# Kernel tuning notes

Measured on AMD Instinct MI355X. Metric: run time of the kernel, lower is better.

## Reference

```python
import jax, jax.numpy as jnp
import numpy as np
from functools import partial


def conv2d(x, w, b, pad):
    # x: [B,C,H,W], w: [O,I,kh,kw]
    out = jax.lax.conv_general_dilated(
        x, w, window_strides=(1, 1), padding=[(pad, pad), (pad, pad)],
        dimension_numbers=("NCHW", "OIHW", "NCHW"))
    return out + b[None, :, None, None]


def maxpool3x3_s1(x):
    return jax.lax.reduce_window(
        x, -jnp.inf, jax.lax.max, (1, 1, 3, 3), (1, 1, 1, 1),
        padding=((0, 0), (0, 0), (1, 1), (1, 1)))


def bilinear_sample(img, y, x):
    # img: [B,C,H,W]; y, x: [B,H,W] float sample coords. Zero outside bounds.
    def one(im, yy, xx):  # im [C,H,W]
        H, W = im.shape[1], im.shape[2]
        y0 = jnp.floor(yy)
        x0 = jnp.floor(xx)
        wy = yy - y0
        wx = xx - x0
        y0i = y0.astype(jnp.int32)
        x0i = x0.astype(jnp.int32)

        def g(yi, xi):
            valid = (yi >= 0) & (yi < H) & (xi >= 0) & (xi < W)
            yc = jnp.clip(yi, 0, H - 1)
            xc = jnp.clip(xi, 0, W - 1)
            return im[:, yc, xc] * valid[None].astype(im.dtype)

        return (g(y0i, x0i) * ((1 - wy) * (1 - wx))[None]
                + g(y0i, x0i + 1) * ((1 - wy) * wx)[None]
                + g(y0i + 1, x0i) * (wy * (1 - wx))[None]
                + g(y0i + 1, x0i + 1) * (wy * wx)[None])

    return jax.vmap(one)(img, y, x)


def deform_conv2d(x, offset, weight, bias, k, pad):
    # torchvision-style: offset [B, 2*k*k, H, W], pairs are (dy, dx) in
    # row-major kernel order. stride=1, dilation=1.
    B, C, H, W = x.shape
    off = offset.reshape(B, k * k, 2, H, W)
    hh = jnp.arange(H, dtype=x.dtype)[None, :, None]  # [1,H,1]
    ww = jnp.arange(W, dtype=x.dtype)[None, None, :]  # [1,1,W]
    out = jnp.zeros((B, weight.shape[0], H, W), x.dtype)
    for t in range(k * k):
        i, j = t // k, t % k
        y = hh + (i - pad) + off[:, t, 0]  # [B,H,W]
        xc = ww + (j - pad) + off[:, t, 1]
        s = bilinear_sample(x, y, xc)      # [B,C,H,W]
        out = out + jnp.einsum("bchw,oc->bohw", s, weight[:, :, i, j])
    return out + bias[None, :, None, None]


def _mk(key, shape, scale=0.05):
    return jax.random.normal(key, shape, dtype=jnp.float32) * scale


def setup_inputs() -> dict:
    key = jax.random.key(0)
    ks = jax.random.split(key, 20)
    C = 512
    Cb = C // 4  # 128
    B, H, W = 8, 64, 64
    return {
        "x": jax.random.normal(ks[0], (B, C, H, W), dtype=jnp.float32),
        "w_b1": _mk(ks[1], (Cb, C, 1, 1)), "b_b1": jnp.zeros((Cb,), jnp.float32),
        "w_b21": _mk(ks[2], (Cb, C, 1, 1)), "b_b21": jnp.zeros((Cb,), jnp.float32),
        "w_off2": _mk(ks[3], (18, Cb, 3, 3), 0.01), "b_off2": jnp.zeros((18,), jnp.float32),
        "w_ddc2": _mk(ks[4], (Cb, Cb, 3, 3)), "b_ddc2": jnp.zeros((Cb,), jnp.float32),
        "w_b31": _mk(ks[5], (Cb, C, 1, 1)), "b_b31": jnp.zeros((Cb,), jnp.float32),
        "w_off3": _mk(ks[6], (50, Cb, 5, 5), 0.01), "b_off3": jnp.zeros((50,), jnp.float32),
        "w_ddc3": _mk(ks[7], (Cb, Cb, 5, 5)), "b_ddc3": jnp.zeros((Cb,), jnp.float32),
        "w_b4": _mk(ks[8], (Cb, C, 1, 1)), "b_b4": jnp.zeros((Cb,), jnp.float32),
        "w_cc": _mk(ks[9], (C, Cb * 4, 1, 1)), "b_cc": jnp.zeros((C,), jnp.float32),
    }


def reference(x, w_b1, b_b1, w_b21, b_b21, w_off2, b_off2, w_ddc2, b_ddc2,
              w_b31, b_b31, w_off3, b_off3, w_ddc3, b_ddc3, w_b4, b_b4,
              w_cc, b_cc):
    b1 = conv2d(x, w_b1, b_b1, 0)

    b2i = conv2d(x, w_b21, b_b21, 0)
    off2 = conv2d(b2i, w_off2, b_off2, 1)
    b2 = deform_conv2d(b2i, off2, w_ddc2, b_ddc2, k=3, pad=1)

    b3i = conv2d(x, w_b31, b_b31, 0)
    off3 = conv2d(b3i, w_off3, b_off3, 2)
    b3 = deform_conv2d(b3i, off3, w_ddc3, b_ddc3, k=5, pad=2)

    b4 = conv2d(maxpool3x3_s1(x), w_b4, b_b4, 0)

    cat = jnp.concatenate([b1, b2, b3, b4], axis=1) * x
    fused = conv2d(cat, w_cc, b_cc, 0)
    return x + jax.nn.sigmoid(fused)
```

## Files before the change

kernel.cpp:

```cpp
#include <hip/hip_runtime.h>
#include <math.h>

#define HW 4096
typedef short short8 __attribute__((ext_vector_type(8)));
typedef float floatx4 __attribute__((ext_vector_type(4)));

#define O_XBT   0ull
#define O_PXB   33554432ull
#define O_CATB  67108864ull
#define O_WPB   100663296ull
#define O_W4B   101056512ull
#define O_WCCB  101187584ull
#define O_WD2T  101711872ull
#define O_WD3T  102006784ull
#define O_WO2T  102825984ull
#define O_WO3T  102973440ull
#define O_T2B   33554432ull
#define O_T3B   41943040ull
#define O_OFF2  50331648ull
#define O_OFF3  52690944ull

__device__ __forceinline__ unsigned short f2b(float f) {
    union { float f; unsigned u; } v; v.f = f;
    unsigned r = v.u + 0x7FFFu + ((v.u >> 16) & 1u);
    return (unsigned short)(r >> 16);
}
__device__ __forceinline__ float lou(unsigned u) {
    union { unsigned u; float f; } v; v.u = u << 16; return v.f;
}
__device__ __forceinline__ float hiu(unsigned u) {
    union { unsigned u; float f; } v; v.u = u & 0xFFFF0000u; return v.f;
}
__device__ __forceinline__ unsigned pk2(float lo, float hi) {
    return (unsigned)f2b(lo) | ((unsigned)f2b(hi) << 16);
}

__global__ __launch_bounds__(256) void k_prepw(
        const float* __restrict__ w1, const float* __restrict__ w21,
        const float* __restrict__ w31, const float* __restrict__ w4,
        const float* __restrict__ wcc, const float* __restrict__ wd2,
        const float* __restrict__ wd3, const float* __restrict__ wo2,
        const float* __restrict__ wo3, unsigned short* __restrict__ ws8) {
    unsigned i = blockIdx.x * 256 + threadIdx.x;
    unsigned short* wpb  = ws8 + (O_WPB  >> 1);
    unsigned short* w4b  = ws8 + (O_W4B  >> 1);
    unsigned short* wccb = ws8 + (O_WCCB >> 1);
    unsigned short* wd2t = ws8 + (O_WD2T >> 1);
    unsigned short* wd3t = ws8 + (O_WD3T >> 1);
    unsigned short* wo2t = ws8 + (O_WO2T >> 1);
    unsigned short* wo3t = ws8 + (O_WO3T >> 1);
    if (i < 196608) {
        int o = i >> 9;
        float v = (o < 128) ? w1[i] : (o < 256) ? w21[i - 65536] : w31[i - 131072];
        wpb[i] = f2b(v);
    } else if (i < 262144) {
        unsigned j = i - 196608; w4b[j] = f2b(w4[j]);
    } else if (i < 524288) {
        unsigned j = i - 262144; wccb[j] = f2b(wcc[j]);
    } else if (i < 671744) {
        unsigned j = i - 524288; int t = j >> 14, o = (j >> 7) & 127, c = j & 127;
        wd2t[j] = f2b(wd2[((o * 128 + c) * 9) + t]);
    } else if (i < 1081344) {
        unsigned j = i - 671744; int t = j >> 14, o = (j >> 7) & 127, c = j & 127;
        wd3t[j] = f2b(wd3[((o * 128 + c) * 25) + t]);
    } else if (i < 1155072) {
        unsigned j = i - 1081344; int t = j >> 13, o = (j >> 7) & 63, c = j & 127;
        wo2t[j] = (o < 18) ? f2b(wo2[((o * 128 + c) * 9) + t]) : 0;
    } else if (i < 1359872) {
        unsigned j = i - 1155072; int t = j >> 13, o = (j >> 7) & 63, c = j & 127;
        wo3t[j] = (o < 50) ? f2b(wo3[((o * 128 + c) * 25) + t]) : 0;
    }
}

__global__ __launch_bounds__(256) void k_xpose(const float* __restrict__ X,
                                               unsigned short* __restrict__ xbT) {
    __shared__ unsigned short t[32][33];
    const int p0 = blockIdx.x * 32, c0 = blockIdx.y * 32, b = blockIdx.z;
    const int tid = threadIdx.x;
    #pragma unroll
    for (int s = 0; s < 4; ++s) {
        int cl = s * 8 + (tid >> 5), pl = tid & 31;
        t[cl][pl] = f2b(X[((size_t)b * 512 + c0 + cl) * HW + p0 + pl]);
    }
    __syncthreads();
    #pragma unroll
    for (int s = 0; s < 4; ++s) {
        int pl = s * 8 + (tid >> 5), cl = tid & 31;
        xbT[((size_t)b * HW + p0 + pl) * 512 + c0 + cl] = t[cl][pl];
    }
}

__global__ __launch_bounds__(256) void k_pool(const unsigned short* __restrict__ xbT,
                                              unsigned short* __restrict__ pxb) {
    unsigned gid = blockIdx.x * 256 + threadIdx.x;
    int b = gid >> 18;
    unsigned rem = gid & 262143;
    int pos = rem >> 6;
    int cg = (rem & 63) * 8;
    int h = pos >> 6, w = pos & 63;
    const unsigned short* img = xbT + (size_t)b * HW * 512;
    float m[8] = {-INFINITY, -INFINITY, -INFINITY, -INFINITY,
                  -INFINITY, -INFINITY, -INFINITY, -INFINITY};
    #pragma unroll
    for (int dy = -1; dy <= 1; ++dy) {
        int hh = h + dy;
        if (hh < 0 || hh >= 64) continue;
        #pragma unroll
        for (int dx = -1; dx <= 1; ++dx) {
            int ww = w + dx;
            if (ww < 0 || ww >= 64) continue;
            uint4 v = *(const uint4*)(img + ((size_t)(hh * 64 + ww)) * 512 + cg);
            unsigned uu[4] = {v.x, v.y, v.z, v.w};
            #pragma unroll
            for (int e = 0; e < 4; ++e) {
                m[2 * e]     = fmaxf(m[2 * e],     lou(uu[e]));
                m[2 * e + 1] = fmaxf(m[2 * e + 1], hiu(uu[e]));
            }
        }
    }
    uint4 o;
    o.x = pk2(m[0], m[1]); o.y = pk2(m[2], m[3]);
    o.z = pk2(m[4], m[5]); o.w = pk2(m[6], m[7]);
    *(uint4*)(pxb + ((size_t)b * HW + pos) * 512 + cg) = o;
}

#define SA(r,c) SM[(r)*40 + (c)]
#define SB(r,c) SM[5120 + (r)*40 + (c)]
#define SC(r,c) SM[(r)*136 + (c)]
__global__ __launch_bounds__(256) void k_gemm(
        const unsigned short* __restrict__ A, const float* __restrict__ bias,
        const unsigned short* __restrict__ Bm,
        unsigned short* __restrict__ dst, int dStride, int dOff) {
    __shared__ unsigned short SM[17408];
    const int tid = threadIdx.x;
    const int n0 = blockIdx.x * 128;
    const int b = blockIdx.z;
    const int wave = tid >> 6, lane = tid & 63, quad = lane >> 4, lr = lane & 15;
    const int m0w = (wave & 1) * 64, n0w = (wave >> 1) * 64;
    const int srow = tid >> 1, skh = (tid & 1) * 16;
    floatx4 acc[4][4] = {};

    for (int k0 = 0; k0 < 512; k0 += 32) {
        const unsigned short* ga = A + (size_t)srow * 512 + k0 + skh;
        uint4 a0 = *(const uint4*)(ga);
        uint4 a1 = *(const uint4*)(ga + 8);
        const unsigned short* gb = Bm + ((size_t)b * HW + n0 + srow) * 512 + k0 + skh;
        uint4 b0 = *(const uint4*)(gb);
        uint4 b1 = *(const uint4*)(gb + 8);
        __syncthreads();
        *(uint4*)&SA(srow, skh) = a0;
        *(uint4*)&SA(srow, skh + 8) = a1;
        *(uint4*)&SB(srow, skh) = b0;
        *(uint4*)&SB(srow, skh + 8) = b1;
        __syncthreads();
        short8 af[4], bf[4];
        #pragma unroll
        for (int i = 0; i < 4; ++i) af[i] = *(short8*)&SA(m0w + i * 16 + lr, quad * 8);
        #pragma unroll
        for (int j = 0; j < 4; ++j) bf[j] = *(short8*)&SB(n0w + j * 16 + lr, quad * 8);
        #pragma unroll
        for (int i = 0; i < 4; ++i)
            #pragma unroll
            for (int j = 0; j < 4; ++j)
                acc[i][j] = __builtin_amdgcn_mfma_f32_16x16x32_bf16(af[i], bf[j], acc[i][j], 0, 0, 0);
    }
    __syncthreads();
    #pragma unroll
    for (int i = 0; i < 4; ++i) {
        float4 bs = *(const float4*)&bias[m0w + i * 16 + quad * 4];
        #pragma unroll
        for (int j = 0; j < 4; ++j) {
            floatx4 v = acc[i][j];
            int pos = n0w + j * 16 + lr;
            int ch = m0w + i * 16 + quad * 4;
            uint2 st;
            st.x = pk2(v[0] + bs.x, v[1] + bs.y);
            st.y = pk2(v[2] + bs.z, v[3] + bs.w);
            *(uint2*)&SC(pos, ch) = st;
        }
    }
    __syncthreads();
    #pragma unroll
    for (int r = 0; r < 8; ++r) {
        int pos = (tid >> 4) + r * 16;
        *(uint4*)&dst[((size_t)b * HW + n0 + pos) * dStride + dOff + (tid & 15) * 8] =
            *(uint4*)&SC(pos, (tid & 15) * 8);
    }
}

template<int KS, int OCH>
__global__ __launch_bounds__(512) void k_offconv2(
        const unsigned short* __restrict__ img,
        const unsigned short* __restrict__ woT,
        const float* __restrict__ bias, float* __restrict__ Out) {
    constexpr int PAD = KS / 2;
    constexpr int TT = KS * KS;
    constexpr int SR = 2 + 2 * PAD;
    constexpr int SC2 = 64 + 2 * PAD;
    constexpr int NE = SR * SC2;
    __shared__ unsigned short slab[NE * 36];
    __shared__ float ctile[64 * 132];
    const int tid = threadIdx.x;
    const int p0 = blockIdx.x * 128, hrow0 = blockIdx.x * 2, b = blockIdx.z;
    const int wave = tid >> 6, lane = tid & 63, quad = lane >> 4, lr = lane & 15;
    const int wm = wave & 1, wn = wave >> 1;
    const unsigned short* ib = img + (size_t)b * HW * 128;
    floatx4 acc[2][2] = {};

    for (int c0 = 0; c0 < 128; c0 += 32) {
        __syncthreads();
        if (tid < NE) {
            int s = tid / SC2, cl = tid % SC2;
            int r = hrow0 - PAD + s, cc = cl - PAD;
            uint4 v0 = {}, v1 = {}, v2 = {}, v3 = {};
            if ((unsigned)r < 64u && (unsigned)cc < 64u) {
                const uint4* g = (const uint4*)(ib + ((size_t)(r * 64 + cc)) * 128 + c0);
                v0 = g[0]; v1 = g[1]; v2 = g[2]; v3 = g[3];
            }
            uint2* d2 = (uint2*)&slab[tid * 36];
            d2[0] = make_uint2(v0.x, v0.y); d2[1] = make_uint2(v0.z, v0.w);
            d2[2] = make_uint2(v1.x, v1.y); d2[3] = make_uint2(v1.z, v1.w);
            d2[4] = make_uint2(v2.x, v2.y); d2[5] = make_uint2(v2.z, v2.w);
            d2[6] = make_uint2(v3.x, v3.y); d2[7] = make_uint2(v3.z, v3.w);
        }
        __syncthreads();
        #pragma unroll
        for (int t = 0; t < TT; ++t) {
            const int ky = t / KS, kx = t % KS;
            short8 af[2], bf[2];
            #pragma unroll
            for (int i = 0; i < 2; ++i)
                af[i] = *(const short8*)&woT[((size_t)t * 64 + wm * 32 + i * 16 + lr) * 128
                                             + c0 + quad * 8];
            #pragma unroll
            for (int j = 0; j < 2; ++j) {
                int p = wn * 32 + j * 16 + lr;
                int e = ((p >> 6) + ky) * SC2 + (p & 63) + kx;
                union { uint2 u[2]; short8 s; } bb;
                const uint2* sp = (const uint2*)&slab[e * 36 + quad * 8];
                bb.u[0] = sp[0]; bb.u[1] = sp[1];
                bf[j] = bb.s;
            }
            #pragma unroll
            for (int i = 0; i < 2; ++i)
                #pragma unroll
                for (int j = 0; j < 2; ++j)
                    acc[i][j] = __builtin_amdgcn_mfma_f32_16x16x32_bf16(af[i], bf[j], acc[i][j], 0, 0, 0);
        }
    }
    __syncthreads();
    #pragma unroll
    for (int i = 0; i < 2; ++i)
        #pragma unroll
        for (int j = 0; j < 2; ++j) {
            floatx4 v = acc[i][j];
            int p = wn * 32 + j * 16 + lr;
            int o = wm * 32 + i * 16 + quad * 4;
            #pragma unroll
            for (int rg = 0; rg < 4; ++rg)
                ctile[(o + rg) * 132 + p] = v[rg];
        }
    __syncthreads();
    {
        int o = tid >> 3, seg = tid & 7;
        if (o < OCH) {
            float bs = bias[o];
            const float* src = &ctile[o * 132 + seg * 16];
            float* dst = &Out[((size_t)b * OCH + o) * HW + p0 + seg * 16];
            #pragma unroll
            for (int q = 0; q < 4; ++q) {
                float4 v = *(const float4*)(src + q * 4);
                v.x += bs; v.y += bs; v.z += bs; v.w += bs;
                *(float4*)(dst + q * 4) = v;
            }
        }
    }
}

template<int KS>
__global__ __launch_bounds__(512) void k_deform4(
        const unsigned short* __restrict__ img,
        const float* __restrict__ Off,
        const unsigned short* __restrict__ wdT,
        const float* __restrict__ bias,
        unsigned short* __restrict__ catb, int dOff) {
    constexpr int PAD = KS / 2;
    constexpr int TT = KS * KS;
    __shared__ unsigned short sW[128][136];
    __shared__ unsigned short sS[128][136];
    const int tid = threadIdx.x;
    const int hrow0 = blockIdx.x * 2, b = blockIdx.z;
    const int wave = tid >> 6, lane = tid & 63, quad = lane >> 4, lr = lane & 15;
    const int m0w = (wave & 1) * 64, n0w = (wave >> 1) * 32;
    const int pos = tid >> 2, cq = (tid & 3) * 32;
    const int pglob = blockIdx.x * 128 + pos;
    const int h = hrow0 + (pos >> 6), w = pos & 63;
    const unsigned short* ib = img + (size_t)b * HW * 128;
    const float* offb = Off + (size_t)b * 2 * TT * HW;
    floatx4 acc[4][2] = {};

    for (int t = 0; t < TT; ++t) {
        float dy = offb[(size_t)(2 * t) * HW + pglob];
        float dx = offb[(size_t)(2 * t + 1) * HW + pglob];
        float fy = (float)(h + t / KS - PAD) + dy;
        float fx = (float)(w + t % KS - PAD) + dx;
        float y0f = floorf(fy), x0f = floorf(fx);
        float wy = fy - y0f, wx = fx - x0f;
        int y0 = (int)y0f, x0 = (int)x0f;
        float w00 = (1.f - wy) * (1.f - wx), w01 = (1.f - wy) * wx;
        float w10 = wy * (1.f - wx), w11 = wy * wx;
        const uint4* wsrc = (const uint4*)(wdT + ((size_t)t * 128 + (tid >> 2)) * 128 + cq);
        uint4 wv[4] = {wsrc[0], wsrc[1], wsrc[2], wsrc[3]};
        bool yv0 = (unsigned)y0 < 64u, yv1 = (unsigned)(y0 + 1) < 64u;
        bool xv0 = (unsigned)x0 < 64u, xv1 = (unsigned)(x0 + 1) < 64u;
        uint4 cA[4] = {}, cB[4] = {}, cC[4] = {}, cD[4] = {};
        long bidx = (long)(y0 * 64 + x0) * 128 + cq;
        if (yv0 && xv0) { const uint4* p = (const uint4*)(ib + bidx);
            cA[0]=p[0]; cA[1]=p[1]; cA[2]=p[2]; cA[3]=p[3]; }
        if (yv0 && xv1) { const uint4* p = (const uint4*)(ib + bidx + 128);
            cB[0]=p[0]; cB[1]=p[1]; cB[2]=p[2]; cB[3]=p[3]; }
        if (yv1 && xv0) { const uint4* p = (const uint4*)(ib + bidx + 64 * 128);
            cC[0]=p[0]; cC[1]=p[1]; cC[2]=p[2]; cC[3]=p[3]; }
        if (yv1 && xv1) { const uint4* p = (const uint4*)(ib + bidx + 65 * 128);
            cD[0]=p[0]; cD[1]=p[1]; cD[2]=p[2]; cD[3]=p[3]; }
        uint4 outv[4];
        #pragma unroll
        for (int j = 0; j < 4; ++j) {
            unsigned a[4] = {cA[j].x, cA[j].y, cA[j].z, cA[j].w};
            unsigned bb[4] = {cB[j].x, cB[j].y, cB[j].z, cB[j].w};
            unsigned c[4] = {cC[j].x, cC[j].y, cC[j].z, cC[j].w};
            unsigned d[4] = {cD[j].x, cD[j].y, cD[j].z, cD[j].w};
            unsigned r[4];
            #pragma unroll
            for (int e = 0; e < 4; ++e) {
                float lo = w00 * lou(a[e]) + w01 * lou(bb[e]) + w10 * lou(c[e]) + w11 * lou(d[e]);
                float hi = w00 * hiu(a[e]) + w01 * hiu(bb[e]) + w10 * hiu(c[e]) + w11 * hiu(d[e]);
                r[e] = pk2(lo, hi);
            }
            outv[j].x = r[0]; outv[j].y = r[1]; outv[j].z = r[2]; outv[j].w = r[3];
        }
        __syncthreads();
        #pragma unroll
        for (int j = 0; j < 4; ++j) {
            *(uint4*)&sW[tid >> 2][cq + j * 8] = wv[j];
            *(uint4*)&sS[pos][cq + j * 8] = outv[j];
        }
        __syncthreads();
        #pragma unroll
        for (int ks = 0; ks < 4; ++ks) {
            short8 af[4], bf[2];
            #pragma unroll
            for (int i = 0; i < 4; ++i)
                af[i] = *(short8*)&sW[m0w + i * 16 + lr][ks * 32 + quad * 8];
            #pragma unroll
            for (int j = 0; j < 2; ++j)
                bf[j] = *(short8*)&sS[n0w + j * 16 + lr][ks * 32 + quad * 8];
            #pragma unroll
            for (int i = 0; i < 4; ++i)
                #pragma unroll
                for (int j = 0; j < 2; ++j)
                    acc[i][j] = __builtin_amdgcn_mfma_f32_16x16x32_bf16(af[i], bf[j], acc[i][j], 0, 0, 0);
        }
    }
    __syncthreads();
    #pragma unroll
    for (int i = 0; i < 4; ++i) {
        float4 bs = *(const float4*)&bias[m0w + i * 16 + quad * 4];
        #pragma unroll
        for (int j = 0; j < 2; ++j) {
            floatx4 v = acc[i][j];
            int p = n0w + j * 16 + lr;
            int ch = m0w + i * 16 + quad * 4;
            uint2 st;
            st.x = pk2(v[0] + bs.x, v[1] + bs.y);
            st.y = pk2(v[2] + bs.z, v[3] + bs.w);
            *(uint2*)&sW[p][ch] = st;
        }
    }
    __syncthreads();
    #pragma unroll
    for (int r = 0; r < 4; ++r) {
        int p = (tid >> 4) + r * 32;
        *(uint4*)&catb[((size_t)b * HW + blockIdx.x * 128 + p) * 512 + dOff + (tid & 15) * 8] =
            *(uint4*)&sW[p][(tid & 15) * 8];
    }
}

__global__ __launch_bounds__(256) void k_gemm_final(
        const unsigned short* __restrict__ A, const float* __restrict__ bias,
        const unsigned short* __restrict__ catb, const unsigned short* __restrict__ xbT,
        const float* __restrict__ X, float* __restrict__ OutF) {
    __shared__ unsigned short sA[128][40];
    __shared__ unsigned short sB[128][40];
    const int tid = threadIdx.x;
    const int n0 = blockIdx.x * 128;
    const int o0 = blockIdx.y * 128;
    const int b = blockIdx.z;
    const int wave = tid >> 6, lane = tid & 63, quad = lane >> 4, lr = lane & 15;
    const int m0w = (wave & 1) * 64, n0w = (wave >> 1) * 64;
    const int srow = tid >> 1, skh = (tid & 1) * 16;
    floatx4 acc[4][4] = {};

    for (int k0 = 0; k0 < 512; k0 += 32) {
        const unsigned short* ga = A + (size_t)(o0 + srow) * 512 + k0 + skh;
        uint4 a0 = *(const uint4*)(ga);
        uint4 a1 = *(const uint4*)(ga + 8);
        size_t bi = ((size_t)b * HW + n0 + srow) * 512 + k0 + skh;
        uint4 c0 = *(const uint4*)(catb + bi);
        uint4 c1 = *(const uint4*)(catb + bi + 8);
        uint4 x0 = *(const uint4*)(xbT + bi);
        uint4 x1 = *(const uint4*)(xbT + bi + 8);
        unsigned cu[8] = {c0.x, c0.y, c0.z, c0.w, c1.x, c1.y, c1.z, c1.w};
        unsigned xu[8] = {x0.x, x0.y, x0.z, x0.w, x1.x, x1.y, x1.z, x1.w};
        unsigned mu[8];
        #pragma unroll
        for (int e = 0; e < 8; ++e)
            mu[e] = pk2(lou(cu[e]) * lou(xu[e]), hiu(cu[e]) * hiu(xu[e]));
        __syncthreads();
        *(uint4*)&sA[srow][skh] = a0;
        *(uint4*)&sA[srow][skh + 8] = a1;
        uint4 m0v; m0v.x = mu[0]; m0v.y = mu[1]; m0v.z = mu[2]; m0v.w = mu[3];
        uint4 m1v; m1v.x = mu[4]; m1v.y = mu[5]; m1v.z = mu[6]; m1v.w = mu[7];
        *(uint4*)&sB[srow][skh] = m0v;
        *(uint4*)&sB[srow][skh + 8] = m1v;
        __syncthreads();
        short8 af[4], bf[4];
        #pragma unroll
        for (int i = 0; i < 4; ++i) af[i] = *(short8*)&sA[m0w + i * 16 + lr][quad * 8];
        #pragma unroll
        for (int j = 0; j < 4; ++j) bf[j] = *(short8*)&sB[n0w + j * 16 + lr][quad * 8];
        #pragma unroll
        for (int i = 0; i < 4; ++i)
            #pragma unroll
            for (int j = 0; j < 4; ++j)
                acc[i][j] = __builtin_amdgcn_mfma_f32_16x16x32_bf16(af[i], bf[j], acc[i][j], 0, 0, 0);
    }
    #pragma unroll
    for (int i = 0; i < 4; ++i) {
        float4 bs = *(const float4*)&bias[o0 + m0w + i * 16 + quad * 4];
        float bsa[4] = {bs.x, bs.y, bs.z, bs.w};
        #pragma unroll
        for (int j = 0; j < 4; ++j) {
            floatx4 v = acc[i][j];
            int pos = n0 + n0w + j * 16 + lr;
            #pragma unroll
            for (int rg = 0; rg < 4; ++rg) {
                int o = o0 + m0w + i * 16 + quad * 4 + rg;
                float f = v[rg] + bsa[rg];
                float sg = 1.f / (1.f + __expf(-f));
                size_t idx = ((size_t)b * 512 + o) * HW + pos;
                OutF[idx] = X[idx] + sg;
            }
        }
    }
}

extern "C" void kernel_launch(void* const* d_in, const int* in_sizes, int n_in,
                              void* d_out, int out_size, void* d_ws, size_t ws_size,
                              hipStream_t stream) {
    const float* x      = (const float*)d_in[0];
    const float* w_b1   = (const float*)d_in[1];
    const float* b_b1   = (const float*)d_in[2];
    const float* w_b21  = (const float*)d_in[3];
    const float* b_b21  = (const float*)d_in[4];
    const float* w_off2 = (const float*)d_in[5];
    const float* b_off2 = (const float*)d_in[6];
    const float* w_ddc2 = (const float*)d_in[7];
    const float* b_ddc2 = (const float*)d_in[8];
    const float* w_b31  = (const float*)d_in[9];
    const float* b_b31  = (const float*)d_in[10];
    const float* w_off3 = (const float*)d_in[11];
    const float* b_off3 = (const float*)d_in[12];
    const float* w_ddc3 = (const float*)d_in[13];
    const float* b_ddc3 = (const float*)d_in[14];
    const float* w_b4   = (const float*)d_in[15];
    const float* b_b4   = (const float*)d_in[16];
    const float* w_cc   = (const float*)d_in[17];
    const float* b_cc   = (const float*)d_in[18];

    char* wsb = (char*)d_ws;
    unsigned short* ws8  = (unsigned short*)d_ws;
    unsigned short* xbT  = (unsigned short*)(wsb + O_XBT);
    unsigned short* pxb  = (unsigned short*)(wsb + O_PXB);
    unsigned short* catb = (unsigned short*)(wsb + O_CATB);
    unsigned short* wpb  = (unsigned short*)(wsb + O_WPB);
    unsigned short* w4b  = (unsigned short*)(wsb + O_W4B);
    unsigned short* wccb = (unsigned short*)(wsb + O_WCCB);
    unsigned short* wd2t = (unsigned short*)(wsb + O_WD2T);
    unsigned short* wd3t = (unsigned short*)(wsb + O_WD3T);
    unsigned short* wo2t = (unsigned short*)(wsb + O_WO2T);
    unsigned short* wo3t = (unsigned short*)(wsb + O_WO3T);
    unsigned short* t2b  = (unsigned short*)(wsb + O_T2B);
    unsigned short* t3b  = (unsigned short*)(wsb + O_T3B);
    float* off2 = (float*)(wsb + O_OFF2);
    float* off3 = (float*)(wsb + O_OFF3);
    float* out  = (float*)d_out;

    k_prepw<<<dim3(5312), dim3(256), 0, stream>>>(
        w_b1, w_b21, w_b31, w_b4, w_cc, w_ddc2, w_ddc3, w_off2, w_off3, ws8);
    k_xpose<<<dim3(128, 16, 8), dim3(256), 0, stream>>>(x, xbT);
    k_pool<<<dim3(8192), dim3(256), 0, stream>>>(xbT, pxb);
    k_gemm<<<dim3(32, 1, 8), dim3(256), 0, stream>>>(w4b, b_b4, pxb, catb, 512, 384);
    k_gemm<<<dim3(32, 1, 8), dim3(256), 0, stream>>>(wpb, b_b1, xbT, catb, 512, 0);
    k_gemm<<<dim3(32, 1, 8), dim3(256), 0, stream>>>(wpb + 128 * 512, b_b21, xbT, t2b, 128, 0);
    k_gemm<<<dim3(32, 1, 8), dim3(256), 0, stream>>>(wpb + 256 * 512, b_b31, xbT, t3b, 128, 0);
    k_offconv2<3, 18><<<dim3(32, 1, 8), dim3(512), 0, stream>>>(t2b, wo2t, b_off2, off2);
    k_offconv2<5, 50><<<dim3(32, 1, 8), dim3(512), 0, stream>>>(t3b, wo3t, b_off3, off3);
    k_deform4<3><<<dim3(32, 1, 8), dim3(512), 0, stream>>>(t2b, off2, wd2t, b_ddc2, catb, 128);
    k_deform4<5><<<dim3(32, 1, 8), dim3(512), 0, stream>>>(t3b, off3, wd3t, b_ddc3, catb, 256);
    k_gemm_final<<<dim3(32, 4, 8), dim3(256), 0, stream>>>(wccb, b_cc, catb, xbT, x, out);
}
```

Before: 554.9 us.

## Shrink deform conv tiles to 32 pixels and prefetch next tap's gathers

The deformable conv kernel now works on 32-pixel tiles with 256 threads instead of 128-pixel tiles with 512 threads, which gives four times as many blocks. A launch bound of 3 blocks per SM is requested. The bilinear gathers and weight loads for tap t+1 are issued before the MFMA work of tap t, and the offsets are read one tap further ahead, so global memory latency overlaps with compute. The costs are more weight traffic per pixel, since every block reloads all the weights for every tap, and higher register pressure from the prefetched data.

After: 800.3 us. +44.2%, slower.

```diff
diff --git a/kernel.cpp b/kernel.cpp
--- a/kernel.cpp
+++ b/kernel.cpp
@@ -278,7 +278,7 @@
 }
 
 template<int KS>
-__global__ __launch_bounds__(512) void k_deform4(
+__global__ __launch_bounds__(256, 3) void k_deform5(
         const unsigned short* __restrict__ img,
         const float* __restrict__ Off,
         const unsigned short* __restrict__ wdT,
@@ -287,76 +287,106 @@
     constexpr int PAD = KS / 2;
     constexpr int TT = KS * KS;
     __shared__ unsigned short sW[128][136];
-    __shared__ unsigned short sS[128][136];
+    __shared__ unsigned short sS[32][136];
     const int tid = threadIdx.x;
-    const int hrow0 = blockIdx.x * 2, b = blockIdx.z;
+    const int b = blockIdx.z;
+    const int p0 = blockIdx.x * 32;
     const int wave = tid >> 6, lane = tid & 63, quad = lane >> 4, lr = lane & 15;
-    const int m0w = (wave & 1) * 64, n0w = (wave >> 1) * 32;
-    const int pos = tid >> 2, cq = (tid & 3) * 32;
-    const int pglob = blockIdx.x * 128 + pos;
-    const int h = hrow0 + (pos >> 6), w = pos & 63;
+    const int m0w = wave * 32;
+    const int pos = tid >> 3;
+    const int cseg = (tid & 7) * 16;
+    const int pglob = p0 + pos;
+    const int h = pglob >> 6, w = pglob & 63;
     const unsigned short* ib = img + (size_t)b * HW * 128;
     const float* offb = Off + (size_t)b * 2 * TT * HW;
-    floatx4 acc[4][2] = {};
-
-    for (int t = 0; t < TT; ++t) {
-        float dy = offb[(size_t)(2 * t) * HW + pglob];
-        float dx = offb[(size_t)(2 * t + 1) * HW + pglob];
+    floatx4 acc[2][2] = {};
+
+    uint4 wv[8];
+    uint4 cn[8];
+    float w00, w01, w10, w11;
+
+    auto ADDR = [&](int t, float dy, float dx) {
         float fy = (float)(h + t / KS - PAD) + dy;
         float fx = (float)(w + t % KS - PAD) + dx;
         float y0f = floorf(fy), x0f = floorf(fx);
         float wy = fy - y0f, wx = fx - x0f;
         int y0 = (int)y0f, x0 = (int)x0f;
-        float w00 = (1.f - wy) * (1.f - wx), w01 = (1.f - wy) * wx;
-        float w10 = wy * (1.f - wx), w11 = wy * wx;
-        const uint4* wsrc = (const uint4*)(wdT + ((size_t)t * 128 + (tid >> 2)) * 128 + cq);
-        uint4 wv[4] = {wsrc[0], wsrc[1], wsrc[2], wsrc[3]};
+        w00 = (1.f - wy) * (1.f - wx); w01 = (1.f - wy) * wx;
+        w10 = wy * (1.f - wx);         w11 = wy * wx;
         bool yv0 = (unsigned)y0 < 64u, yv1 = (unsigned)(y0 + 1) < 64u;
         bool xv0 = (unsigned)x0 < 64u, xv1 = (unsigned)(x0 + 1) < 64u;
-        uint4 cA[4] = {}, cB[4] = {}, cC[4] = {}, cD[4] = {};
-        long bidx = (long)(y0 * 64 + x0) * 128 + cq;
+        long bidx = (long)(y0 * 64 + x0) * 128 + cseg;
+        #pragma unroll
+        for (int q = 0; q < 8; ++q) cn[q] = make_uint4(0u, 0u, 0u, 0u);
         if (yv0 && xv0) { const uint4* p = (const uint4*)(ib + bidx);
-            cA[0]=p[0]; cA[1]=p[1]; cA[2]=p[2]; cA[3]=p[3]; }
+            cn[0] = p[0]; cn[1] = p[1]; }
         if (yv0 && xv1) { const uint4* p = (const uint4*)(ib + bidx + 128);
-            cB[0]=p[0]; cB[1]=p[1]; cB[2]=p[2]; cB[3]=p[3]; }
-        if (yv1 && xv0) { const uint4* p = (const uint4*)(ib + bidx + 64 * 128);
-            cC[0]=p[0]; cC[1]=p[1]; cC[2]=p[2]; cC[3]=p[3]; }
-        if (yv1 && xv1) { const uint4* p = (const uint4*)(ib + bidx + 65 * 128);
-            cD[0]=p[0]; cD[1]=p[1]; cD[2]=p[2]; cD[3]=p[3]; }
-        uint4 outv[4];
-        #pragma unroll
-        for (int j = 0; j < 4; ++j) {
-            unsigned a[4] = {cA[j].x, cA[j].y, cA[j].z, cA[j].w};
-            unsigned bb[4] = {cB[j].x, cB[j].y, cB[j].z, cB[j].w};
-            unsigned c[4] = {cC[j].x, cC[j].y, cC[j].z, cC[j].w};
-            unsigned d[4] = {cD[j].x, cD[j].y, cD[j].z, cD[j].w};
-            unsigned r[4];
-            #pragma unroll
-            for (int e = 0; e < 4; ++e) {
-                float lo = w00 * lou(a[e]) + w01 * lou(bb[e]) + w10 * lou(c[e]) + w11 * lou(d[e]);
-                float hi = w00 * hiu(a[e]) + w01 * hiu(bb[e]) + w10 * hiu(c[e]) + w11 * hiu(d[e]);
-                r[e] = pk2(lo, hi);
-            }
-            outv[j].x = r[0]; outv[j].y = r[1]; outv[j].z = r[2]; outv[j].w = r[3];
-        }
-        __syncthreads();
-        #pragma unroll
-        for (int j = 0; j < 4; ++j) {
-            *(uint4*)&sW[tid >> 2][cq + j * 8] = wv[j];
-            *(uint4*)&sS[pos][cq + j * 8] = outv[j];
-        }
-        __syncthreads();
+            cn[2] = p[0]; cn[3] = p[1]; }
+        if (yv1 && xv0) { const uint4* p = (const uint4*)(ib + bidx + 8192);
+            cn[4] = p[0]; cn[5] = p[1]; }
+        if (yv1 && xv1) { const uint4* p = (const uint4*)(ib + bidx + 8320);
+            cn[6] = p[0]; cn[7] = p[1]; }
+        const uint4* wsrc = (const uint4*)(wdT + ((size_t)t * 128 + (tid >> 1)) * 128
+                                           + (tid & 1) * 64);
+        #pragma unroll
+        for (int q = 0; q < 8; ++q) wv[q] = wsrc[q];
+    };
+
+    {
+        float coy = offb[pglob];
+        float cox = offb[HW + pglob];
+        ADDR(0, coy, cox);
+    }
+    float noy = 0.f, nox = 0.f;
+    if (TT > 1) { noy = offb[2 * HW + pglob]; nox = offb[3 * HW + pglob]; }
+
+    for (int t = 0; t < TT; ++t) {
+        uint4 s0, s1;
+        {
+            unsigned r[8];
+            #pragma unroll
+            for (int g = 0; g < 2; ++g) {
+                unsigned au[4] = {cn[g].x,     cn[g].y,     cn[g].z,     cn[g].w};
+                unsigned bu[4] = {cn[2 + g].x, cn[2 + g].y, cn[2 + g].z, cn[2 + g].w};
+                unsigned cu[4] = {cn[4 + g].x, cn[4 + g].y, cn[4 + g].z, cn[4 + g].w};
+                unsigned du[4] = {cn[6 + g].x, cn[6 + g].y, cn[6 + g].z, cn[6 + g].w};
+                #pragma unroll
+                for (int e = 0; e < 4; ++e) {
+                    float lo = w00 * lou(au[e]) + w01 * lou(bu[e])
+                             + w10 * lou(cu[e]) + w11 * lou(du[e]);
+                    float hi = w00 * hiu(au[e]) + w01 * hiu(bu[e])
+                             + w10 * hiu(cu[e]) + w11 * hiu(du[e]);
+                    r[g * 4 + e] = pk2(lo, hi);
+                }
+            }
+            s0 = make_uint4(r[0], r[1], r[2], r[3]);
+            s1 = make_uint4(r[4], r[5], r[6], r[7]);
+        }
+        __syncthreads();
+        #pragma unroll
+        for (int q = 0; q < 8; ++q)
+            *(uint4*)&sW[tid >> 1][(tid & 1) * 64 + q * 8] = wv[q];
+        *(uint4*)&sS[pos][cseg] = s0;
+        *(uint4*)&sS[pos][cseg + 8] = s1;
+        __syncthreads();
+        if (t + 1 < TT) {
+            ADDR(t + 1, noy, nox);
+            if (t + 2 < TT) {
+                noy = offb[(size_t)(2 * t + 4) * HW + pglob];
+                nox = offb[(size_t)(2 * t + 5) * HW + pglob];
+            }
+        }
         #pragma unroll
         for (int ks = 0; ks < 4; ++ks) {
-            short8 af[4], bf[2];
-            #pragma unroll
-            for (int i = 0; i < 4; ++i)
+            short8 af[2], bf[2];
+            #pragma unroll
+            for (int i = 0; i < 2; ++i)
                 af[i] = *(short8*)&sW[m0w + i * 16 + lr][ks * 32 + quad * 8];
             #pragma unroll
             for (int j = 0; j < 2; ++j)
-                bf[j] = *(short8*)&sS[n0w + j * 16 + lr][ks * 32 + quad * 8];
-            #pragma unroll
-            for (int i = 0; i < 4; ++i)
+                bf[j] = *(short8*)&sS[j * 16 + lr][ks * 32 + quad * 8];
+            #pragma unroll
+            for (int i = 0; i < 2; ++i)
                 #pragma unroll
                 for (int j = 0; j < 2; ++j)
                     acc[i][j] = __builtin_amdgcn_mfma_f32_16x16x32_bf16(af[i], bf[j], acc[i][j], 0, 0, 0);
@@ -364,25 +394,26 @@
     }
     __syncthreads();
     #pragma unroll
-    for (int i = 0; i < 4; ++i) {
+    for (int i = 0; i < 2; ++i) {
         float4 bs = *(const float4*)&bias[m0w + i * 16 + quad * 4];
         #pragma unroll
         for (int j = 0; j < 2; ++j) {
             floatx4 v = acc[i][j];
-            int p = n0w + j * 16 + lr;
+            int p = j * 16 + lr;
             int ch = m0w + i * 16 + quad * 4;
             uint2 st;
             st.x = pk2(v[0] + bs.x, v[1] + bs.y);
             st.y = pk2(v[2] + bs.z, v[3] + bs.w);
-            *(uint2*)&sW[p][ch] = st;
-        }
-    }
-    __syncthreads();
-    #pragma unroll
-    for (int r = 0; r < 4; ++r) {
-        int p = (tid >> 4) + r * 32;
-        *(uint4*)&catb[((size_t)b * HW + blockIdx.x * 128 + p) * 512 + dOff + (tid & 15) * 8] =
-            *(uint4*)&sW[p][(tid & 15) * 8];
+            *(uint2*)&sS[p][ch] = st;
+        }
+    }
+    __syncthreads();
+    #pragma unroll
+    for (int r = 0; r < 2; ++r) {
+        int idx = r * 256 + tid;
+        int p = idx >> 4, sg = (idx & 15) * 8;
+        *(uint4*)&catb[((size_t)b * HW + p0 + p) * 512 + dOff + sg] =
+            *(uint4*)&sS[p][sg];
     }
 }
 
@@ -506,7 +537,7 @@
     k_gemm<<<dim3(32, 1, 8), dim3(256), 0, stream>>>(wpb + 256 * 512, b_b31, xbT, t3b, 128, 0);
     k_offconv2<3, 18><<<dim3(32, 1, 8), dim3(512), 0, stream>>>(t2b, wo2t, b_off2, off2);
     k_offconv2<5, 50><<<dim3(32, 1, 8), dim3(512), 0, stream>>>(t3b, wo3t, b_off3, off3);
-    k_deform4<3><<<dim3(32, 1, 8), dim3(512), 0, stream>>>(t2b, off2, wd2t, b_ddc2, catb, 128);
-    k_deform4<5><<<dim3(32, 1, 8), dim3(512), 0, stream>>>(t3b, off3, wd3t, b_ddc3, catb, 256);
+    k_deform5<3><<<dim3(128, 1, 8), dim3(256), 0, stream>>>(t2b, off2, wd2t, b_ddc2, catb, 128);
+    k_deform5<5><<<dim3(128, 1, 8), dim3(256), 0, stream>>>(t3b, off3, wd3t, b_ddc3, catb, 256);
     k_gemm_final<<<dim3(32, 4, 8), dim3(256), 0, stream>>>(wccb, b_cc, catb, xbT, x, out);
 }
```
